# Kernel optimization log

Hardware: AMD Instinct MI355X
Metric: run time of the kernel (lower is better)

## Reference

```python
import jax, jax.numpy as jnp
import numpy as np

NBINS = 256
RGB_W = jnp.array([0.2989, 0.5870, 0.1140], dtype=jnp.float32)  # tf.image.rgb_to_grayscale weights


def _otsu_threshold(g):
    # g: [H, W] grayscale image. skimage-style Otsu: 256 bins over [min, max].
    mn = g.min()
    mx = g.max()
    rng = jnp.maximum(mx - mn, 1e-12)
    idx = jnp.clip(((g - mn) * (NBINS / rng)).astype(jnp.int32), 0, NBINS - 1)
    hist = jnp.zeros((NBINS,), jnp.float32).at[idx.ravel()].add(1.0)
    centers = mn + (jnp.arange(NBINS, dtype=jnp.float32) + 0.5) * (rng / NBINS)
    # class-1: bins [0..t], class-2: bins (t..255]
    w1 = jnp.cumsum(hist)                              # [256]
    w2 = jnp.cumsum(hist[::-1])[::-1]                  # [256]
    hc = hist * centers
    m1 = jnp.cumsum(hc) / jnp.maximum(w1, 1e-12)
    m2 = (jnp.cumsum(hc[::-1]) / jnpveps(w2))[::-1] if False else (jnp.cumsum(hc[::-1]) / jnp.maximum(jnp.cumsum(hist[::-1]), 1e-12))[::-1]
    var12 = w1[:-1] * w2[1:] * (m1[:-1] - m2[1:]) ** 2  # between-class variance, [255]
    return centers[jnp.argmax(var12)]


def setup_inputs() -> dict:
    key = jax.random.key(0)
    x = jax.random.uniform(key, (64, 512, 512, 3), dtype=jnp.float32) * 255.0
    return {"x": x}


def reference(x):
    # grayscale: [B, H, W]
    gray = jnp.einsum("bhwc,c->bhw", x, RGB_W)
    thr = jax.vmap(_otsu_threshold)(gray)              # [B]
    binary = jnp.where(gray > thr[:, None, None], 255.0, 0.0)  # [B, H, W]
    # grayscale_to_rgb: tile channel
    return jnp.broadcast_to(binary[..., None], binary.shape + (3,))
```

## Files before the change

kernel.cpp:

```cpp
#include <hip/hip_runtime.h>
#include <stdint.h>

#define NBINS 256
#define HW    (512 * 512)
#define NIMG  64
#define MMB   64
#define HB    32
#define RB 0
#define GB 1032
#define BB 2064
#define STW 3096

__device__ __forceinline__ double gray_of(float r, float g, float b) {
    return fma((double)b, (double)0.1140f,
           fma((double)g, (double)0.5870f,
               (double)r * (double)0.2989f));
}

__device__ __forceinline__ void stage3(const float4* __restrict__ xv, int64_t tile4,
                                       float* __restrict__ st, int tid) {
    #pragma unroll
    for (int k = 0; k < 3; ++k) {
        const int q = k * 256 + tid;
        const float4 v = xv[tile4 + q];
        const int f0 = q * 4;
        int p = (int)(((unsigned)f0 * 21846u) >> 16);
        int c = f0 - 3 * p;
        const float e[4] = {v.x, v.y, v.z, v.w};
        #pragma unroll
        for (int j = 0; j < 4; ++j) {
            const int base = (c == 0) ? RB : ((c == 1) ? GB : BB);
            st[base + p] = e[j];
            if (++c == 3) { c = 0; ++p; }
        }
    }
}

__global__ __launch_bounds__(256) void k_minmax(const float* __restrict__ x,
                                                double* __restrict__ mm_part) {
    __shared__ float st[STW];
    __shared__ double smn[4], smx[4];
    const int tid = threadIdx.x;
    const int img = blockIdx.x >> 6;
    const int blk = blockIdx.x & 63;
    const int64_t img4 = (int64_t)img * (HW * 3 / 4);
    const float4* xv = (const float4*)x;
    double mn = 1e300, mx = -1e300;
    for (int it = 0; it < 4; ++it) {
        stage3(xv, img4 + (int64_t)(blk * 4 + it) * 768, st, tid);
        __syncthreads();
        const float4 R = *(const float4*)&st[RB + 4 * tid];
        const float4 G = *(const float4*)&st[GB + 4 * tid];
        const float4 B = *(const float4*)&st[BB + 4 * tid];
        const double g0 = gray_of(R.x, G.x, B.x), g1 = gray_of(R.y, G.y, B.y),
                     g2 = gray_of(R.z, G.z, B.z), g3 = gray_of(R.w, G.w, B.w);
        mn = fmin(mn, fmin(fmin(g0, g1), fmin(g2, g3)));
        mx = fmax(mx, fmax(fmax(g0, g1), fmax(g2, g3)));
        __syncthreads();
    }
    #pragma unroll
    for (int off = 32; off; off >>= 1) {
        mn = fmin(mn, __shfl_xor(mn, off));
        mx = fmax(mx, __shfl_xor(mx, off));
    }
    if ((tid & 63) == 0) { smn[tid >> 6] = mn; smx[tid >> 6] = mx; }
    __syncthreads();
    if (tid == 0) {
        mn = fmin(fmin(smn[0], smn[1]), fmin(smn[2], smn[3]));
        mx = fmax(fmax(smx[0], smx[1]), fmax(smx[2], smx[3]));
        mm_part[(img * MMB + blk) * 2 + 0] = mn;
        mm_part[(img * MMB + blk) * 2 + 1] = mx;
    }
}

__device__ __forceinline__ void mm_reduce(const double* __restrict__ mm_part, int img,
                                          int tid, double* __restrict__ sdm) {
    if (tid < 64) {
        double mn = mm_part[(img * MMB + tid) * 2 + 0];
        double mx = mm_part[(img * MMB + tid) * 2 + 1];
        #pragma unroll
        for (int off = 32; off; off >>= 1) {
            mn = fmin(mn, __shfl_xor(mn, off));
            mx = fmax(mx, __shfl_xor(mx, off));
        }
        if (tid == 0) { sdm[0] = mn; sdm[1] = mx; }
    }
}

template <bool WIDX>
__global__ __launch_bounds__(256) void k_hist(const float* __restrict__ x,
        const double* __restrict__ mm_part,
        unsigned* __restrict__ hist_part, unsigned* __restrict__ idx4) {
    __shared__ float st[STW];
    __shared__ unsigned lh[NBINS];
    __shared__ double sdm[2];
    const int tid = threadIdx.x;
    const int img = blockIdx.x >> 5;
    const int blk = blockIdx.x & 31;
    lh[tid] = 0u;
    mm_reduce(mm_part, img, tid, sdm);
    __syncthreads();
    const double mn = sdm[0];
    const double scale = 256.0 / fmax(__dsub_rn(sdm[1], mn), 1e-12);
    const int64_t img4 = (int64_t)img * (HW * 3 / 4);
    const float4* xv = (const float4*)x;
    for (int it = 0; it < 8; ++it) {
        stage3(xv, img4 + (int64_t)(blk * 8 + it) * 768, st, tid);
        __syncthreads();
        const float4 R = *(const float4*)&st[RB + 4 * tid];
        const float4 G = *(const float4*)&st[GB + 4 * tid];
        const float4 B = *(const float4*)&st[BB + 4 * tid];
        const double g[4] = {gray_of(R.x, G.x, B.x), gray_of(R.y, G.y, B.y),
                             gray_of(R.z, G.z, B.z), gray_of(R.w, G.w, B.w)};
        unsigned pack = 0;
        #pragma unroll
        for (int j = 0; j < 4; ++j) {
            int id = (int)__dmul_rn(__dsub_rn(g[j], mn), scale);
            id = id < 0 ? 0 : (id > 255 ? 255 : id);
            atomicAdd(&lh[id], 1u);
            pack |= (unsigned)id << (8 * j);
        }
        if (WIDX) idx4[img * (HW / 4) + (blk * 8 + it) * 256 + tid] = pack;
        __syncthreads();
    }
    hist_part[(img * HB + blk) * NBINS + tid] = lh[tid];
}

__global__ void k_otsu(const unsigned* __restrict__ hist_part,
                       const double* __restrict__ mm_part,
                       double* __restrict__ thr, int* __restrict__ bidx) {
    __shared__ double h[NBINS], w2s[NBINS], m2s[NBINS], vv[NBINS];
    __shared__ double sdm[2];
    const int img = blockIdx.x, t = threadIdx.x;
    mm_reduce(mm_part, img, t, sdm);
    unsigned hu = 0;
    for (int b = 0; b < HB; ++b) hu += hist_part[(img * HB + b) * NBINS + t];
    h[t] = (double)hu;
    __syncthreads();
    const double mn   = sdm[0];
    const double rng  = fmax(__dsub_rn(sdm[1], mn), 1e-12);
    const double step = rng / 256.0;
    double w1 = 0.0, hc1 = 0.0;
    for (int j = 0; j <= t; ++j) {
        const double c = __dadd_rn(mn, __dmul_rn((double)j + 0.5, step));
        w1  = __dadd_rn(w1, h[j]);
        hc1 = __dadd_rn(hc1, __dmul_rn(h[j], c));
    }
    const double m1 = hc1 / fmax(w1, 1e-12);
    double w2 = 0.0, hc2 = 0.0;
    for (int j = NBINS - 1; j >= t; --j) {
        const double c = __dadd_rn(mn, __dmul_rn((double)j + 0.5, step));
        w2  = __dadd_rn(w2, h[j]);
        hc2 = __dadd_rn(hc2, __dmul_rn(h[j], c));
    }
    w2s[t] = w2;
    m2s[t] = hc2 / fmax(w2, 1e-12);
    __syncthreads();
    if (t < NBINS - 1) {
        const double d = __dsub_rn(m1, m2s[t + 1]);
        vv[t] = __dmul_rn(__dmul_rn(w1, w2s[t + 1]), __dmul_rn(d, d));
    }
    __syncthreads();
    if (t == 0) {
        double best = -1.0; int bi = 0;
        for (int i = 0; i < NBINS - 1; ++i)
            if (vv[i] > best) { best = vv[i]; bi = i; }
        thr[img]  = __dadd_rn(mn, __dmul_rn((double)bi + 0.5, step));
        bidx[img] = bi;
    }
}

template <bool UIDX>
__global__ __launch_bounds__(256) void k_binarize(const float* __restrict__ x,
        const unsigned* __restrict__ idx4,
        const double* __restrict__ thr, const int* __restrict__ bidx,
        float* __restrict__ out) {
    __shared__ float st[STW];
    __shared__ float bst[1024];
    const int tid = threadIdx.x;
    const int img = blockIdx.x >> 6;
    const int blk = blockIdx.x & 63;
    const double T = thr[img];
    const int bi = UIDX ? bidx[img] : 0;
    const int64_t img4 = (int64_t)img * (HW * 3 / 4);
    const float4* xv = (const float4*)x;
    float4* ov = (float4*)out;
    for (int it = 0; it < 4; ++it) {
        const int tl = blk * 4 + it;
        float bb[4];
        if (UIDX) {
            const unsigned pk = idx4[img * (HW / 4) + tl * 256 + tid];
            #pragma unroll
            for (int j = 0; j < 4; ++j) {
                const int id = (pk >> (8 * j)) & 255;
                float r;
                if (id > bi)      r = 255.f;
                else if (id < bi) r = 0.f;
                else {
                    const int64_t p = (int64_t)img * HW + (int64_t)tl * 1024 + 4 * tid + j;
                    const double g = gray_of(x[3 * p], x[3 * p + 1], x[3 * p + 2]);
                    r = (g > T) ? 255.f : 0.f;
                }
                bb[j] = r;
            }
        } else {
            stage3(xv, img4 + (int64_t)tl * 768, st, tid);
            __syncthreads();
            const float4 R = *(const float4*)&st[RB + 4 * tid];
            const float4 G = *(const float4*)&st[GB + 4 * tid];
            const float4 B = *(const float4*)&st[BB + 4 * tid];
            bb[0] = (gray_of(R.x, G.x, B.x) > T) ? 255.f : 0.f;
            bb[1] = (gray_of(R.y, G.y, B.y) > T) ? 255.f : 0.f;
            bb[2] = (gray_of(R.z, G.z, B.z) > T) ? 255.f : 0.f;
            bb[3] = (gray_of(R.w, G.w, B.w) > T) ? 255.f : 0.f;
        }
        *(float4*)&bst[4 * tid] = make_float4(bb[0], bb[1], bb[2], bb[3]);
        __syncthreads();
        const int64_t ob4 = img4 + (int64_t)tl * 768;
        #pragma unroll
        for (int k = 0; k < 3; ++k) {
            const int q  = k * 256 + tid;
            const int p0 = (int)(((unsigned)(q * 4) * 21846u) >> 16);
            const int m  = q - 3 * (int)(((unsigned)q * 21846u) >> 16);
            const float lo = bst[p0];
            const float hi = bst[p0 + 1 < 1024 ? p0 + 1 : 1023];
            float4 o;
            o.x = lo;
            o.y = (m + 1 >= 3) ? hi : lo;
            o.z = (m + 2 >= 3) ? hi : lo;
            o.w = (m + 3 >= 3) ? hi : lo;
            ov[ob4 + q] = o;
        }
        __syncthreads();
    }
}

extern "C" void kernel_launch(void* const* d_in, const int* in_sizes, int n_in,
                              void* d_out, int out_size, void* d_ws, size_t ws_size,
                              hipStream_t stream) {
    const float* x = (const float*)d_in[0];
    float* out = (float*)d_out;
    uint8_t* ws = (uint8_t*)d_ws;

    double*   thr       = (double*)(ws);
    int*      bidx      = (int*)(ws + 512);
    double*   mm_part   = (double*)(ws + 1024);
    unsigned* hist_part = (unsigned*)(ws + 66560);
    unsigned* idx4      = (unsigned*)(ws + 2163712);
    const bool use_idx = ws_size >= (size_t)2163712 + (size_t)NIMG * HW;

    k_minmax<<<NIMG * MMB, 256, 0, stream>>>(x, mm_part);
    if (use_idx) k_hist<true ><<<NIMG * HB, 256, 0, stream>>>(x, mm_part, hist_part, idx4);
    else         k_hist<false><<<NIMG * HB, 256, 0, stream>>>(x, mm_part, hist_part, nullptr);
    k_otsu<<<NIMG, 256, 0, stream>>>(hist_part, mm_part, thr, bidx);
    if (use_idx) k_binarize<true ><<<NIMG * MMB, 256, 0, stream>>>(x, idx4, thr, bidx, out);
    else         k_binarize<false><<<NIMG * MMB, 256, 0, stream>>>(x, nullptr, thr, bidx, out);
}
```

Baseline: 147.1 us.

## Cache 16-bit fixed-point grayscale in minmax pass to skip rereading RGB in hist

The min/max pass now also writes a 16-bit fixed-point grayscale value (gray*256) per pixel to workspace. The histogram pass reads this compact cache instead of restaging the full RGB input, and falls back to reading the original pixel only when the fixed-point interval straddles a bin boundary. Binarization uses the same interval test against the threshold instead of a precomputed bin index. This is meant to cut the global reads of the hist pass from 12 bytes to 2 bytes per pixel, at the cost of extra writes in the minmax pass and scattered fallback loads near bin edges.

Result: faster. 137.0 us (-6.9%).

```diff
diff --git a/kernel.cpp b/kernel.cpp
--- a/kernel.cpp
+++ b/kernel.cpp
@@ -10,6 +10,7 @@
 #define GB 1032
 #define BB 2064
 #define STW 3096
+#define FINV 0.00390625
 
 __device__ __forceinline__ double gray_of(float r, float g, float b) {
     return fma((double)b, (double)0.1140f,
@@ -36,8 +37,10 @@
     }
 }
 
+template <bool WF>
 __global__ __launch_bounds__(256) void k_minmax(const float* __restrict__ x,
-                                                double* __restrict__ mm_part) {
+                                                double* __restrict__ mm_part,
+                                                unsigned long long* __restrict__ fid4) {
     __shared__ float st[STW];
     __shared__ double smn[4], smx[4];
     const int tid = threadIdx.x;
@@ -47,7 +50,8 @@
     const float4* xv = (const float4*)x;
     double mn = 1e300, mx = -1e300;
     for (int it = 0; it < 4; ++it) {
-        stage3(xv, img4 + (int64_t)(blk * 4 + it) * 768, st, tid);
+        const int tl = blk * 4 + it;
+        stage3(xv, img4 + (int64_t)tl * 768, st, tid);
         __syncthreads();
         const float4 R = *(const float4*)&st[RB + 4 * tid];
         const float4 G = *(const float4*)&st[GB + 4 * tid];
@@ -56,6 +60,13 @@
                      g2 = gray_of(R.z, G.z, B.z), g3 = gray_of(R.w, G.w, B.w);
         mn = fmin(mn, fmin(fmin(g0, g1), fmin(g2, g3)));
         mx = fmax(mx, fmax(fmax(g0, g1), fmax(g2, g3)));
+        if (WF) {
+            const unsigned long long f0 = (unsigned long long)(unsigned)(g0 * 256.0);
+            const unsigned long long f1 = (unsigned long long)(unsigned)(g1 * 256.0);
+            const unsigned long long f2 = (unsigned long long)(unsigned)(g2 * 256.0);
+            const unsigned long long f3 = (unsigned long long)(unsigned)(g3 * 256.0);
+            fid4[img * (HW / 4) + tl * 256 + tid] = f0 | (f1 << 16) | (f2 << 32) | (f3 << 48);
+        }
         __syncthreads();
     }
     #pragma unroll
@@ -87,10 +98,15 @@
     }
 }
 
-template <bool WIDX>
-__global__ __launch_bounds__(256) void k_hist(const float* __restrict__ x,
-        const double* __restrict__ mm_part,
-        unsigned* __restrict__ hist_part, unsigned* __restrict__ idx4) {
+__device__ __forceinline__ int bin_of(double g, double mn, double s) {
+    int id = (int)__dmul_rn(__dsub_rn(g, mn), s);
+    return id < 0 ? 0 : (id > 255 ? 255 : id);
+}
+
+template <bool UF>
+__global__ __launch_bounds__(256) void k_hist(const unsigned long long* __restrict__ fid4,
+        const float* __restrict__ x, const double* __restrict__ mm_part,
+        unsigned* __restrict__ hist_part) {
     __shared__ float st[STW];
     __shared__ unsigned lh[NBINS];
     __shared__ double sdm[2];
@@ -101,34 +117,48 @@
     mm_reduce(mm_part, img, tid, sdm);
     __syncthreads();
     const double mn = sdm[0];
-    const double scale = 256.0 / fmax(__dsub_rn(sdm[1], mn), 1e-12);
+    const double s  = 256.0 / fmax(__dsub_rn(sdm[1], mn), 1e-12);
     const int64_t img4 = (int64_t)img * (HW * 3 / 4);
     const float4* xv = (const float4*)x;
     for (int it = 0; it < 8; ++it) {
-        stage3(xv, img4 + (int64_t)(blk * 8 + it) * 768, st, tid);
-        __syncthreads();
-        const float4 R = *(const float4*)&st[RB + 4 * tid];
-        const float4 G = *(const float4*)&st[GB + 4 * tid];
-        const float4 B = *(const float4*)&st[BB + 4 * tid];
-        const double g[4] = {gray_of(R.x, G.x, B.x), gray_of(R.y, G.y, B.y),
-                             gray_of(R.z, G.z, B.z), gray_of(R.w, G.w, B.w)};
-        unsigned pack = 0;
-        #pragma unroll
-        for (int j = 0; j < 4; ++j) {
-            int id = (int)__dmul_rn(__dsub_rn(g[j], mn), scale);
-            id = id < 0 ? 0 : (id > 255 ? 255 : id);
-            atomicAdd(&lh[id], 1u);
-            pack |= (unsigned)id << (8 * j);
-        }
-        if (WIDX) idx4[img * (HW / 4) + (blk * 8 + it) * 256 + tid] = pack;
-        __syncthreads();
-    }
+        const int tl = blk * 8 + it;
+        if (UF) {
+            const unsigned long long pk = fid4[img * (HW / 4) + tl * 256 + tid];
+            #pragma unroll
+            for (int j = 0; j < 4; ++j) {
+                const unsigned f = (unsigned)(pk >> (16 * j)) & 0xFFFFu;
+                const double glo = (double)f * FINV;
+                const double ghi = (double)(f + 1) * FINV;
+                const int clo = bin_of(glo, mn, s);
+                const int chi = bin_of(ghi, mn, s);
+                int id;
+                if (clo == chi) id = clo;
+                else {
+                    const int64_t p = (int64_t)img * HW + (int64_t)tl * 1024 + 4 * tid + j;
+                    id = bin_of(gray_of(x[3 * p], x[3 * p + 1], x[3 * p + 2]), mn, s);
+                }
+                atomicAdd(&lh[id], 1u);
+            }
+        } else {
+            stage3(xv, img4 + (int64_t)tl * 768, st, tid);
+            __syncthreads();
+            const float4 R = *(const float4*)&st[RB + 4 * tid];
+            const float4 G = *(const float4*)&st[GB + 4 * tid];
+            const float4 B = *(const float4*)&st[BB + 4 * tid];
+            atomicAdd(&lh[bin_of(gray_of(R.x, G.x, B.x), mn, s)], 1u);
+            atomicAdd(&lh[bin_of(gray_of(R.y, G.y, B.y), mn, s)], 1u);
+            atomicAdd(&lh[bin_of(gray_of(R.z, G.z, B.z), mn, s)], 1u);
+            atomicAdd(&lh[bin_of(gray_of(R.w, G.w, B.w), mn, s)], 1u);
+            __syncthreads();
+        }
+    }
+    __syncthreads();
     hist_part[(img * HB + blk) * NBINS + tid] = lh[tid];
 }
 
 __global__ void k_otsu(const unsigned* __restrict__ hist_part,
                        const double* __restrict__ mm_part,
-                       double* __restrict__ thr, int* __restrict__ bidx) {
+                       double* __restrict__ thr) {
     __shared__ double h[NBINS], w2s[NBINS], m2s[NBINS], vv[NBINS];
     __shared__ double sdm[2];
     const int img = blockIdx.x, t = threadIdx.x;
@@ -165,15 +195,13 @@
         double best = -1.0; int bi = 0;
         for (int i = 0; i < NBINS - 1; ++i)
             if (vv[i] > best) { best = vv[i]; bi = i; }
-        thr[img]  = __dadd_rn(mn, __dmul_rn((double)bi + 0.5, step));
-        bidx[img] = bi;
-    }
-}
-
-template <bool UIDX>
-__global__ __launch_bounds__(256) void k_binarize(const float* __restrict__ x,
-        const unsigned* __restrict__ idx4,
-        const double* __restrict__ thr, const int* __restrict__ bidx,
+        thr[img] = __dadd_rn(mn, __dmul_rn((double)bi + 0.5, step));
+    }
+}
+
+template <bool UF>
+__global__ __launch_bounds__(256) void k_binarize(const unsigned long long* __restrict__ fid4,
+        const float* __restrict__ x, const double* __restrict__ thr,
         float* __restrict__ out) {
     __shared__ float st[STW];
     __shared__ float bst[1024];
@@ -181,21 +209,22 @@
     const int img = blockIdx.x >> 6;
     const int blk = blockIdx.x & 63;
     const double T = thr[img];
-    const int bi = UIDX ? bidx[img] : 0;
     const int64_t img4 = (int64_t)img * (HW * 3 / 4);
     const float4* xv = (const float4*)x;
     float4* ov = (float4*)out;
     for (int it = 0; it < 4; ++it) {
         const int tl = blk * 4 + it;
         float bb[4];
-        if (UIDX) {
-            const unsigned pk = idx4[img * (HW / 4) + tl * 256 + tid];
+        if (UF) {
+            const unsigned long long pk = fid4[img * (HW / 4) + tl * 256 + tid];
             #pragma unroll
             for (int j = 0; j < 4; ++j) {
-                const int id = (pk >> (8 * j)) & 255;
+                const unsigned f = (unsigned)(pk >> (16 * j)) & 0xFFFFu;
+                const double glo = (double)f * FINV;
+                const double ghi = (double)(f + 1) * FINV;
                 float r;
-                if (id > bi)      r = 255.f;
-                else if (id < bi) r = 0.f;
+                if (glo > T)       r = 255.f;
+                else if (ghi <= T) r = 0.f;
                 else {
                     const int64_t p = (int64_t)img * HW + (int64_t)tl * 1024 + 4 * tid + j;
                     const double g = gray_of(x[3 * p], x[3 * p + 1], x[3 * p + 2]);
@@ -242,17 +271,17 @@
     float* out = (float*)d_out;
     uint8_t* ws = (uint8_t*)d_ws;
 
-    double*   thr       = (double*)(ws);
-    int*      bidx      = (int*)(ws + 512);
-    double*   mm_part   = (double*)(ws + 1024);
-    unsigned* hist_part = (unsigned*)(ws + 66560);
-    unsigned* idx4      = (unsigned*)(ws + 2163712);
-    const bool use_idx = ws_size >= (size_t)2163712 + (size_t)NIMG * HW;
-
-    k_minmax<<<NIMG * MMB, 256, 0, stream>>>(x, mm_part);
-    if (use_idx) k_hist<true ><<<NIMG * HB, 256, 0, stream>>>(x, mm_part, hist_part, idx4);
-    else         k_hist<false><<<NIMG * HB, 256, 0, stream>>>(x, mm_part, hist_part, nullptr);
-    k_otsu<<<NIMG, 256, 0, stream>>>(hist_part, mm_part, thr, bidx);
-    if (use_idx) k_binarize<true ><<<NIMG * MMB, 256, 0, stream>>>(x, idx4, thr, bidx, out);
-    else         k_binarize<false><<<NIMG * MMB, 256, 0, stream>>>(x, nullptr, thr, bidx, out);
-}
+    double*             thr       = (double*)(ws);
+    double*             mm_part   = (double*)(ws + 1024);
+    unsigned*           hist_part = (unsigned*)(ws + 66560);
+    unsigned long long* fid4      = (unsigned long long*)(ws + 2163712);
+    const bool uf = ws_size >= (size_t)2163712 + (size_t)NIMG * HW * 2;
+
+    if (uf) k_minmax<true ><<<NIMG * MMB, 256, 0, stream>>>(x, mm_part, fid4);
+    else    k_minmax<false><<<NIMG * MMB, 256, 0, stream>>>(x, mm_part, nullptr);
+    if (uf) k_hist<true ><<<NIMG * HB, 256, 0, stream>>>(fid4, x, mm_part, hist_part);
+    else    k_hist<false><<<NIMG * HB, 256, 0, stream>>>(nullptr, x, mm_part, hist_part);
+    k_otsu<<<NIMG, 256, 0, stream>>>(hist_part, mm_part, thr);
+    if (uf) k_binarize<true ><<<NIMG * MMB, 256, 0, stream>>>(fid4, x, thr, out);
+    else    k_binarize<false><<<NIMG * MMB, 256, 0, stream>>>(nullptr, x, thr, out);
+}
```
